# Optimization experiments

Measured on AMD Instinct MI355X. Metric: run time of the kernel, lower is better.

Reference implementation:

```python
import jax, jax.numpy as jnp
import numpy as np

D_MODEL = 1024
NHEAD = 16
HEAD_DIM = D_MODEL // NHEAD
SCALE = 1.0 / np.sqrt(HEAD_DIM).astype(np.float32)
B, L = 2, 2048
NEG_INF = -1e30


def setup_inputs() -> dict:
    key = jax.random.key(0)
    ks = jax.random.split(key, 12)
    xav = np.sqrt(6.0 / (D_MODEL + D_MODEL)).astype(np.float32)  # xavier_uniform gain=1
    def lin_w(k):
        return jax.random.uniform(k, (D_MODEL, D_MODEL), jnp.float32, -xav, xav)
    x = jax.random.normal(ks[0], (B, L, D_MODEL), jnp.float32)
    role_mask = jax.random.randint(ks[1], (B, L), 0, 2, jnp.int32)
    # causal attention mask: True = masked (upper triangle above diagonal)
    attn_mask = jnp.triu(jnp.ones((L, L), jnp.bool_), k=1)
    # random key padding: True = padded key
    key_padding_mask = jax.random.randint(ks[2], (B, L), 0, 2, jnp.int32).astype(jnp.bool_)
    return {
        "x": x,
        "role_mask": role_mask,
        "attn_mask": attn_mask,
        "key_padding_mask": key_padding_mask,
        "Wq": lin_w(ks[3]), "bq": jnp.zeros((D_MODEL,), jnp.float32),
        "Wk": lin_w(ks[4]), "bk": jnp.zeros((D_MODEL,), jnp.float32),
        "Wv": lin_w(ks[5]), "bv": jnp.zeros((D_MODEL,), jnp.float32),
        "Wo": lin_w(ks[6]), "bo": jnp.zeros((D_MODEL,), jnp.float32),
        "delta": jnp.asarray(1.0, jnp.float32),
    }


def reference(x, role_mask, attn_mask, key_padding_mask,
              Wq, bq, Wk, bk, Wv, bv, Wo, bo, delta):
    Bb, Ll, Dd = x.shape
    def heads(t):  # [B,L,D] -> [B,H,L,hd]
        return t.reshape(Bb, Ll, NHEAD, HEAD_DIM).transpose(0, 2, 1, 3)
    Q = heads(x @ Wq.T + bq)
    K = heads(x @ Wk.T + bk)
    V = heads(x @ Wv.T + bv)
    scores = jnp.einsum('bhqd,bhkd->bhqk', Q, K) * SCALE  # [B,H,L,L]
    same_role = (role_mask[:, :, None] == role_mask[:, None, :])  # [B,L,L]
    scores = scores + (same_role.astype(scores.dtype) * delta)[:, None, :, :]
    scores = jnp.where(attn_mask[None, None, :, :], -jnp.inf, scores)
    scores = jnp.where(key_padding_mask[:, None, None, :], -jnp.inf, scores)
    attn = jax.nn.softmax(scores, axis=-1)
    attn = jnp.nan_to_num(attn, nan=0.0, posinf=0.0, neginf=0.0)
    out = jnp.einsum('bhqk,bhkd->bhqd', attn, V)
    out = out.transpose(0, 2, 1, 3).reshape(Bb, Ll, Dd)
    return out @ Wo.T + bo
```

## Files before the change

### kernel.cpp

```cpp
#include <hip/hip_runtime.h>
#include <hip/hip_bf16.h>

#define DM 1024
#define NH 16
#define HD 64
#define BB 2
#define LL 2048
#define SCALE 0.125f
#define NEG_BIG -1e30f
#define LOG2E 1.4426950408889634f
#define SC2 (SCALE * LOG2E)
#define FIXM 16.0f
#define SLOTB 8448
#define POOL0_SLOTS 960

typedef __bf16 bf16;
typedef __bf16 bf16x8 __attribute__((ext_vector_type(8)));
typedef __bf16 bf16x4 __attribute__((ext_vector_type(4)));
typedef float f32x4 __attribute__((ext_vector_type(4)));

static __device__ inline bf16x8 load8(const bf16* p) {
    return *reinterpret_cast<const bf16x8*>(p);
}

static __device__ inline float scrub(float x) {
    union { float f; unsigned u; } c; c.f = x;
    return ((c.u & 0x7F800000u) == 0x7F800000u) ? 0.f : x;
}

typedef __attribute__((address_space(1))) const unsigned char ga_t;
typedef __attribute__((address_space(3))) unsigned char ls_t;
static __device__ inline void gload_lds16(const void* g, void* l) {
    __builtin_amdgcn_global_load_lds((ga_t*)g, (ls_t*)l, 16, 0, 0);
}

__global__ __launch_bounds__(256) void prep_all(
    const float* __restrict__ x,
    const float* __restrict__ Wq, const float* __restrict__ Wk,
    const float* __restrict__ Wv, const float* __restrict__ Wo,
    bf16* __restrict__ xb, bf16* __restrict__ Wqb, bf16* __restrict__ Wkb,
    bf16* __restrict__ Wvb, bf16* __restrict__ Wob,
    const int* __restrict__ role, const void* __restrict__ kpad,
    const float* __restrict__ deltap, float2* __restrict__ biasG)
{
    const int tid = threadIdx.x;
    const int gid = blockIdx.x;
    if (gid < 2048) {
        const float* src; bf16* dst; size_t base;
        if (gid < 1024) { src = x; dst = xb; base = (size_t)gid * 1024; }
        else {
            const int wsel = (gid - 1024) >> 8;
            src = (wsel == 0) ? Wq : (wsel == 1) ? Wk : (wsel == 2) ? Wv : Wo;
            dst = (wsel == 0) ? Wqb : (wsel == 1) ? Wkb : (wsel == 2) ? Wvb : Wob;
            base = (size_t)((gid - 1024) & 255) * 1024;
        }
#pragma unroll
        for (int it = 0; it < 4; it++) {
            const size_t i = base + it * 256 + tid;
            const f32x4 v = ((const f32x4*)src)[i];
            bf16x4 o;
            o[0] = (bf16)v[0]; o[1] = (bf16)v[1]; o[2] = (bf16)v[2]; o[3] = (bf16)v[3];
            ((bf16x4*)dst)[i] = o;
        }
        return;
    }
    const unsigned char* kb = (const unsigned char*)kpad;
    int f3F = 0, fLow = 0, fOff = 0;
    for (int i = (tid & 63); i < BB * LL; i += 64) {
        const unsigned char v = kb[i];
        if (v == 0x3F) f3F = 1;
        if ((i & 3) < 2 && v) fLow = 1;
        if ((i & 3) && v) fOff = 1;
    }
    const int mode = __any(f3F) ? (__any(fLow) ? 3 : 2) : (__any(fOff) ? 1 : 0);
    const float d2 = scrub(deltap[0]) * LOG2E;
    const int idx = (gid - 2048) * 256 + tid;
    const bool pad = (mode == 0) ? (((const int*)kpad)[idx] != 0)
                   : (mode == 1) ? (((const unsigned char*)kpad)[idx] != 0)
                   : (mode == 2) ? (((const float*)kpad)[idx] != 0.f)
                                 : (((const unsigned short*)kpad)[idx] != 0);
    const int r = role[idx];
    const float base = (pad ? NEG_BIG : 0.f) - FIXM;
    float2 o;
    o.x = base + ((r == 0) ? d2 : 0.f);
    o.y = base + ((r == 1) ? d2 : 0.f);
    biasG[idx] = o;
}

__global__ __launch_bounds__(256) void qkv_bf16(
    const bf16* __restrict__ xb,
    const bf16* __restrict__ Wqb, const bf16* __restrict__ Wkb, const bf16* __restrict__ Wvb,
    const float* __restrict__ bq, const float* __restrict__ bk, const float* __restrict__ bv,
    bf16* __restrict__ qw, bf16* __restrict__ kw, bf16* __restrict__ vtw)
{
    __shared__ bf16 As[128 * 32];
    __shared__ bf16 Bs[128 * 32];
    const int tid = threadIdx.x;
    const int lane = tid & 63, w = tid >> 6;
    const int wm = w >> 1, wn = w & 1;
    const int ln = lane & 15, quad = lane >> 4;

    const int m0 = blockIdx.x * 128;
    const int sel = blockIdx.y >> 3;
    const int nloc0 = (blockIdx.y & 7) * 128;

    const bf16* Wb = (sel == 0) ? Wqb : ((sel == 1) ? Wkb : Wvb);
    const float* bias = (sel == 0) ? bq : ((sel == 1) ? bk : bv);

    const int rA = lane >> 2;
    const int cA = (lane & 3) * 8;

    f32x4 acc[4][4] = {};
    for (int k0 = 0; k0 < DM; k0 += 32) {
        __syncthreads();
#pragma unroll
        for (int s = 0; s < 2; s++) {
            const int r0 = s * 64 + w * 16;
            gload_lds16(xb + (size_t)(m0 + r0 + rA) * DM + k0 + cA, &As[r0 * 32]);
            gload_lds16(Wb + (size_t)(nloc0 + r0 + rA) * DM + k0 + cA, &Bs[r0 * 32]);
        }
        __syncthreads();
        bf16x8 a[4], b[4];
#pragma unroll
        for (int mi = 0; mi < 4; mi++)
            a[mi] = *(bf16x8*)&As[(wm * 64 + mi * 16 + ln) * 32 + quad * 8];
#pragma unroll
        for (int ni = 0; ni < 4; ni++)
            b[ni] = *(bf16x8*)&Bs[(wn * 64 + ni * 16 + ln) * 32 + quad * 8];
#pragma unroll
        for (int mi = 0; mi < 4; mi++)
#pragma unroll
            for (int ni = 0; ni < 4; ni++)
                acc[mi][ni] = __builtin_amdgcn_mfma_f32_16x16x32_bf16(a[mi], b[ni], acc[mi][ni], 0, 0, 0);
    }

#pragma unroll
    for (int mi = 0; mi < 4; mi++) {
#pragma unroll
        for (int ni = 0; ni < 4; ni++) {
            const int ncol = nloc0 + wn * 64 + ni * 16 + ln;
            const float bv_ = bias[ncol];
            const int hh = ncol >> 6, dd = ncol & 63;
#pragma unroll
            for (int i = 0; i < 4; i++) {
                const int row = m0 + wm * 64 + mi * 16 + quad * 4 + i;
                const int bb = row >> 11, llr = row & (LL - 1);
                const bf16 v = (bf16)scrub(acc[mi][ni][i] + bv_);
                if (sel == 0)
                    qw[(((size_t)(bb * NH + hh) * LL) + llr) * HD + dd] = v;
                else if (sel == 1)
                    kw[(((size_t)(bb * NH + hh) * LL) + llr) * HD + dd] = v;
                else {
                    const int kl = llr & 63;
                    const int pos = (llr & ~63) + ((kl & 15) * 4 + (kl >> 4));
                    vtw[(((size_t)(bb * NH + hh) * HD) + dd) * LL + pos] = v;
                }
            }
        }
    }
}

#define PSTR 36
__global__ __launch_bounds__(256) void attn_v9(
    const bf16* __restrict__ qw, const bf16* __restrict__ kw, const bf16* __restrict__ vtw,
    const int* __restrict__ role, const float2* __restrict__ biasG,
    char* __restrict__ pool0, char* __restrict__ pool1,
    bf16* __restrict__ attn_out)
{
    const int xg = blockIdx.x;
    int qb, c;
    if (xg < 24)      { qb = 31 - xg / 3; c = xg % 3; }
    else if (xg < 48) { qb = 23 - (xg - 24) / 2; c = (xg - 24) % 2; }
    else              { qb = 59 - xg; c = 0; }
    const int nch = (qb + 12) / 12;

    __shared__ bf16 Ks[2][2][64 * 32];
    __shared__ bf16 Vs[2][2][64 * 32];
    __shared__ bf16 Ps[4][2][16 * PSTR];

    const int tid = threadIdx.x;
    const int lane = tid & 63, w = tid >> 6;
    const int col = lane & 15, quad = lane >> 4;
    const int bh = blockIdx.y;
    const int h = bh & (NH - 1), b = bh >> 4;
    const int q0 = qb * 64 + w * 16;

    const bf16* qbase = qw + (size_t)((b * NH + h) * LL) * HD;
    const bf16* kbase = kw + (size_t)((b * NH + h) * LL) * HD;
    const bf16* vbase = vtw + (size_t)((b * NH + h) * HD) * LL;
    const float2* bias2 = biasG + (size_t)b * LL;
    const int* rrow = role + b * LL;

    const int srow = lane >> 2;
    const int scol = (lane & 3) * 8;
    const bf16* ksrc = kbase + (size_t)(w * 16 + srow) * HD + scol;
    const bf16* vsrc = vbase + (size_t)(w * 16 + srow) * LL + scol;

    bf16x8 qf[2];
    qf[0] = load8(qbase + (size_t)(q0 + col) * HD + quad * 8);
    qf[1] = load8(qbase + (size_t)(q0 + col) * HD + 32 + quad * 8);

    int role_q[4];
#pragma unroll
    for (int i = 0; i < 4; i++) role_q[i] = rrow[q0 + quad * 4 + i];

    float lacc[4] = {0.f, 0.f, 0.f, 0.f};
    f32x4 o[4] = {};

    const int t0 = c * 12;
    const int t1 = (t0 + 12 < qb + 1) ? t0 + 12 : qb + 1;

    {
        const int kp = t0 * 64;
#pragma unroll
        for (int st = 0; st < 2; st++)
            gload_lds16(ksrc + (size_t)kp * HD + st * 32, &Ks[0][st][w * 512]);
#pragma unroll
        for (int kh = 0; kh < 2; kh++)
            gload_lds16(vsrc + kp + kh * 32, &Vs[0][kh][w * 512]);
    }

    for (int kt = t0; kt < t1; kt++) {
        const int cur = (kt - t0) & 1;
        __syncthreads();

        if (kt + 1 < t1) {
            const int k1 = (kt + 1) * 64;
#pragma unroll
            for (int st = 0; st < 2; st++)
                gload_lds16(ksrc + (size_t)k1 * HD + st * 32, &Ks[cur ^ 1][st][w * 512]);
#pragma unroll
            for (int kh = 0; kh < 2; kh++)
                gload_lds16(vsrc + k1 + kh * 32, &Vs[cur ^ 1][kh][w * 512]);
        }

        const int k0 = kt * 64;
        float2 bb[4];
#pragma unroll
        for (int ns = 0; ns < 4; ns++) bb[ns] = bias2[k0 + ns * 16 + col];

        f32x4 s[4] = {};
#pragma unroll
        for (int st = 0; st < 2; st++) {
#pragma unroll
            for (int ns = 0; ns < 4; ns++) {
                const bf16x8 kf = *(bf16x8*)&Ks[cur][st][(ns * 16 + col) * 32 + quad * 8];
                s[ns] = __builtin_amdgcn_mfma_f32_16x16x32_bf16(qf[st], kf, s[ns], 0, 0, 0);
            }
        }
        const bool diag = (kt == qb);
        const int half = col >> 3;
        const int poff = (col & 7) * 4;
#pragma unroll
        for (int i = 0; i < 4; i++) {
            bf16x4 pk;
#pragma unroll
            for (int ns = 0; ns < 4; ns++) {
                float sv = fmaf(s[ns][i], SC2, role_q[i] ? bb[ns].y : bb[ns].x);
                if (diag && (k0 + ns * 16 + col) > q0 + quad * 4 + i) sv = NEG_BIG;
                const float p = exp2f(fminf(sv, 14.f));
                lacc[i] += p;
                pk[ns] = (bf16)p;
            }
            *(bf16x4*)&Ps[w][half][(quad * 4 + i) * PSTR + poff] = pk;
        }
        bf16x8 pf[2];
#pragma unroll
        for (int st = 0; st < 2; st++)
            pf[st] = *(bf16x8*)&Ps[w][st][col * PSTR + quad * 8];
#pragma unroll
        for (int ns = 0; ns < 4; ns++) {
#pragma unroll
            for (int kh = 0; kh < 2; kh++) {
                const bf16x8 vf = *(bf16x8*)&Vs[cur][kh][(ns * 16 + col) * 32 + quad * 8];
                o[ns] = __builtin_amdgcn_mfma_f32_16x16x32_bf16(pf[kh], vf, o[ns], 0, 0, 0);
            }
        }
    }

    if (nch == 1) {
        bf16* orow = attn_out + (size_t)(b * LL) * DM;
#pragma unroll
        for (int i = 0; i < 4; i++) {
            float l = lacc[i];
#pragma unroll
            for (int off = 8; off > 0; off >>= 1)
                l += __shfl_xor(l, off, 16);
            const float inv = (l > 0.f) ? 1.f / l : 0.f;
            const int qq = q0 + quad * 4 + i;
#pragma unroll
            for (int ns = 0; ns < 4; ns++)
                orow[(size_t)qq * DM + h * HD + ns * 16 + col] = (bf16)scrub(o[ns][i] * inv);
        }
    } else {
        const int base = (qb <= 23) ? (qb - 12) * 2 : 24 + (qb - 24) * 3;
        const int slot = bh * 48 + base + c;
        char* ptr = (slot < POOL0_SLOTS) ? (pool0 + (size_t)slot * SLOTB)
                                         : (pool1 + (size_t)(slot - POOL0_SLOTS) * SLOTB);
        bf16* op = (bf16*)ptr;
        float* lp = (float*)(ptr + 8192);
#pragma unroll
        for (int i = 0; i < 4; i++) {
            float l = lacc[i];
#pragma unroll
            for (int off = 8; off > 0; off >>= 1)
                l += __shfl_xor(l, off, 16);
            const int r = w * 16 + quad * 4 + i;
            if (col == 0) lp[r] = l;
#pragma unroll
            for (int ns = 0; ns < 4; ns++)
                op[r * 64 + ns * 16 + col] = (bf16)scrub(o[ns][i]);
        }
    }
}

__global__ __launch_bounds__(256) void combine(
    const char* __restrict__ pool0, const char* __restrict__ pool1,
    bf16* __restrict__ attn_out)
{
    const int qb = 12 + blockIdx.x;
    const int bh = blockIdx.y;
    const int h = bh & (NH - 1), b = bh >> 4;
    const int nch = (qb + 12) / 12;
    const int base = (qb <= 23) ? (qb - 12) * 2 : 24 + (qb - 24) * 3;

    const char* ptr[3];
    for (int c = 0; c < nch; c++) {
        const int slot = bh * 48 + base + c;
        ptr[c] = (slot < POOL0_SLOTS) ? (pool0 + (size_t)slot * SLOTB)
                                      : (pool1 + (size_t)(slot - POOL0_SLOTS) * SLOTB);
    }

    __shared__ float linv[64];
    const int tid = threadIdx.x;
    if (tid < 64) {
        float ls = 0.f;
        for (int c = 0; c < nch; c++) ls += ((const float*)(ptr[c] + 8192))[tid];
        linv[tid] = (ls > 0.f) ? 1.f / ls : 0.f;
    }
    __syncthreads();

    const int r = tid >> 2;
    const int d0 = (tid & 3) * 16;
    float acc[16] = {};
    for (int c = 0; c < nch; c++) {
        const bf16* op = (const bf16*)ptr[c];
#pragma unroll
        for (int half = 0; half < 2; half++) {
            const bf16x8 v = load8(op + r * 64 + d0 + half * 8);
#pragma unroll
            for (int j = 0; j < 8; j++) acc[half * 8 + j] += (float)v[j];
        }
    }
    const float inv = linv[r];
    bf16x8 outv[2];
#pragma unroll
    for (int half = 0; half < 2; half++)
#pragma unroll
        for (int j = 0; j < 8; j++)
            outv[half][j] = (bf16)scrub(acc[half * 8 + j] * inv);
    bf16* orow = attn_out + ((size_t)(b * LL) + qb * 64 + r) * DM + h * HD + d0;
    *(bf16x8*)orow = outv[0];
    *(bf16x8*)(orow + 8) = outv[1];
}

__global__ __launch_bounds__(256) void out_bf16(
    const bf16* __restrict__ A, const bf16* __restrict__ Wb,
    const float* __restrict__ bias, float* __restrict__ out)
{
    __shared__ bf16 As[128 * 32];
    __shared__ bf16 Bs[64 * 32];
    const int tid = threadIdx.x;
    const int lane = tid & 63, w = tid >> 6;
    const int ln = lane & 15, quad = lane >> 4;
    const int m0 = blockIdx.x * 128;
    const int n0 = blockIdx.y * 64;

    const int rA = lane >> 2;
    const int cA = (lane & 3) * 8;

    f32x4 acc[2][4] = {};
    for (int k0 = 0; k0 < DM; k0 += 32) {
        __syncthreads();
#pragma unroll
        for (int s = 0; s < 2; s++) {
            const int r0 = s * 64 + w * 16;
            gload_lds16(A + (size_t)(m0 + r0 + rA) * DM + k0 + cA, &As[r0 * 32]);
        }
        gload_lds16(Wb + (size_t)(n0 + w * 16 + rA) * DM + k0 + cA, &Bs[w * 16 * 32]);
        __syncthreads();
        bf16x8 a[2], b[4];
#pragma unroll
        for (int mi = 0; mi < 2; mi++)
            a[mi] = *(bf16x8*)&As[(w * 32 + mi * 16 + ln) * 32 + quad * 8];
#pragma unroll
        for (int ni = 0; ni < 4; ni++)
            b[ni] = *(bf16x8*)&Bs[(ni * 16 + ln) * 32 + quad * 8];
#pragma unroll
        for (int mi = 0; mi < 2; mi++)
#pragma unroll
            for (int ni = 0; ni < 4; ni++)
                acc[mi][ni] = __builtin_amdgcn_mfma_f32_16x16x32_bf16(a[mi], b[ni], acc[mi][ni], 0, 0, 0);
    }
#pragma unroll
    for (int mi = 0; mi < 2; mi++) {
#pragma unroll
        for (int ni = 0; ni < 4; ni++) {
            const int ncol = n0 + ni * 16 + ln;
            const float bv_ = bias[ncol];
#pragma unroll
            for (int i = 0; i < 4; i++) {
                const int row = m0 + w * 32 + mi * 16 + quad * 4 + i;
                out[(size_t)row * DM + ncol] = scrub(acc[mi][ni][i] + bv_);
            }
        }
    }
}

extern "C" void kernel_launch(void* const* d_in, const int* in_sizes, int n_in,
                              void* d_out, int out_size, void* d_ws, size_t ws_size,
                              hipStream_t stream) {
    const float* x    = (const float*)d_in[0];
    const int*   role = (const int*)d_in[1];
    const void*  kpad = d_in[3];
    const float* Wq = (const float*)d_in[4];
    const float* bq = (const float*)d_in[5];
    const float* Wk = (const float*)d_in[6];
    const float* bk = (const float*)d_in[7];
    const float* Wv = (const float*)d_in[8];
    const float* bv = (const float*)d_in[9];
    const float* Wo = (const float*)d_in[10];
    const float* bo = (const float*)d_in[11];
    const float* dl = (const float*)d_in[12];

    char* ws = (char*)d_ws;
    bf16* qw   = (bf16*)(ws);
    bf16* kw   = (bf16*)(ws + (size_t)(8u  << 20));
    bf16* Wqb  = (bf16*)(ws + (size_t)(16u << 20));
    bf16* Wkb  = (bf16*)(ws + (size_t)(18u << 20));
    bf16* Wvb  = (bf16*)(ws + (size_t)(20u << 20));
    char* pool0 = ws + (size_t)(16u << 20);
    bf16* aw   = (bf16*)(ws + (size_t)(24u << 20));
    bf16* vtw  = (bf16*)(ws + (size_t)(32u << 20));
    bf16* xb   = (bf16*)(ws + (size_t)(40u << 20));
    char* pool1 = ws + (size_t)(40u << 20);
    bf16* Wob  = (bf16*)(ws + (size_t)(48u << 20) + 65536);
    float2* biasG = (float2*)(ws + (size_t)(48u << 20));
    float* out = (float*)d_out;

    prep_all<<<dim3(2064), dim3(256), 0, stream>>>(
        x, Wq, Wk, Wv, Wo, xb, Wqb, Wkb, Wvb, Wob, role, kpad, dl, biasG);
    qkv_bf16<<<dim3(32, 24), dim3(256), 0, stream>>>(
        xb, Wqb, Wkb, Wvb, bq, bk, bv, qw, kw, vtw);
    attn_v9<<<dim3(60, 32), dim3(256), 0, stream>>>(
        qw, kw, vtw, role, biasG, pool0, pool1, aw);
    combine<<<dim3(20, 32), dim3(256), 0, stream>>>(pool0, pool1, aw);
    out_bf16<<<dim3(32, 16), dim3(256), 0, stream>>>(aw, Wob, bo, out);
}
```

Baseline: 246.3 us.

## Fuse split-KV combine into attention via atomic tickets and XOR-swizzle LDS tiles

Removes the separate combine kernel. Each split-KV attention block now takes an atomic ticket, and the last block to finish for a query tile reduces the partial outputs and writes the normalized result. The tickets are zeroed in the prep kernel. Separately, LDS tiles in the QKV GEMM, the output GEMM and the attention K/V staging use an XOR swizzle of the 16-byte column chunk by row, meant to cut bank conflicts on the MFMA fragment reads. This saves one launch and its tail, at the cost of threadfences and atomics in the attention kernel.

```diff
diff --git a/kernel.cpp b/kernel.cpp
--- a/kernel.cpp
+++ b/kernel.cpp
@@ -34,6 +34,7 @@
     __builtin_amdgcn_global_load_lds((ga_t*)g, (ls_t*)l, 16, 0, 0);
 }
 
+
 __global__ __launch_bounds__(256) void prep_all(
     const float* __restrict__ x,
     const float* __restrict__ Wq, const float* __restrict__ Wk,
@@ -41,7 +42,8 @@
     bf16* __restrict__ xb, bf16* __restrict__ Wqb, bf16* __restrict__ Wkb,
     bf16* __restrict__ Wvb, bf16* __restrict__ Wob,
     const int* __restrict__ role, const void* __restrict__ kpad,
-    const float* __restrict__ deltap, float2* __restrict__ biasG)
+    const float* __restrict__ deltap, float2* __restrict__ biasG,
+    int* __restrict__ tickets)
 {
     const int tid = threadIdx.x;
     const int gid = blockIdx.x;
@@ -75,6 +77,7 @@
     const int mode = __any(f3F) ? (__any(fLow) ? 3 : 2) : (__any(fOff) ? 1 : 0);
     const float d2 = scrub(deltap[0]) * LOG2E;
     const int idx = (gid - 2048) * 256 + tid;
+    if (idx < 640) tickets[idx] = 0;
     const bool pad = (mode == 0) ? (((const int*)kpad)[idx] != 0)
                    : (mode == 1) ? (((const unsigned char*)kpad)[idx] != 0)
                    : (mode == 2) ? (((const float*)kpad)[idx] != 0.f)
@@ -108,7 +111,7 @@
     const float* bias = (sel == 0) ? bq : ((sel == 1) ? bk : bv);
 
     const int rA = lane >> 2;
-    const int cA = (lane & 3) * 8;
+    const int cA = (((lane & 3) ^ (rA & 3)) * 8);
 
     f32x4 acc[4][4] = {};
     for (int k0 = 0; k0 < DM; k0 += 32) {
@@ -122,11 +125,15 @@
         __syncthreads();
         bf16x8 a[4], b[4];
 #pragma unroll
-        for (int mi = 0; mi < 4; mi++)
-            a[mi] = *(bf16x8*)&As[(wm * 64 + mi * 16 + ln) * 32 + quad * 8];
-#pragma unroll
-        for (int ni = 0; ni < 4; ni++)
-            b[ni] = *(bf16x8*)&Bs[(wn * 64 + ni * 16 + ln) * 32 + quad * 8];
+        for (int mi = 0; mi < 4; mi++) {
+            const int row = wm * 64 + mi * 16 + ln;
+            a[mi] = *(bf16x8*)&As[row * 32 + ((quad ^ (row & 3)) * 8)];
+        }
+#pragma unroll
+        for (int ni = 0; ni < 4; ni++) {
+            const int row = wn * 64 + ni * 16 + ln;
+            b[ni] = *(bf16x8*)&Bs[row * 32 + ((quad ^ (row & 3)) * 8)];
+        }
 #pragma unroll
         for (int mi = 0; mi < 4; mi++)
 #pragma unroll
@@ -161,10 +168,11 @@
 }
 
 #define PSTR 36
-__global__ __launch_bounds__(256) void attn_v9(
+__global__ __launch_bounds__(256) void attn_v10(
     const bf16* __restrict__ qw, const bf16* __restrict__ kw, const bf16* __restrict__ vtw,
     const int* __restrict__ role, const float2* __restrict__ biasG,
     char* __restrict__ pool0, char* __restrict__ pool1,
+    int* __restrict__ tickets,
     bf16* __restrict__ attn_out)
 {
     const int xg = blockIdx.x;
@@ -177,6 +185,8 @@
     __shared__ bf16 Ks[2][2][64 * 32];
     __shared__ bf16 Vs[2][2][64 * 32];
     __shared__ bf16 Ps[4][2][16 * PSTR];
+    __shared__ float linv[64];
+    __shared__ int amLast;
 
     const int tid = threadIdx.x;
     const int lane = tid & 63, w = tid >> 6;
@@ -192,7 +202,7 @@
     const int* rrow = role + b * LL;
 
     const int srow = lane >> 2;
-    const int scol = (lane & 3) * 8;
+    const int scol = (((lane & 3) ^ (srow & 3)) * 8);
     const bf16* ksrc = kbase + (size_t)(w * 16 + srow) * HD + scol;
     const bf16* vsrc = vbase + (size_t)(w * 16 + srow) * LL + scol;
 
@@ -244,7 +254,8 @@
         for (int st = 0; st < 2; st++) {
 #pragma unroll
             for (int ns = 0; ns < 4; ns++) {
-                const bf16x8 kf = *(bf16x8*)&Ks[cur][st][(ns * 16 + col) * 32 + quad * 8];
+                const int row = ns * 16 + col;
+                const bf16x8 kf = *(bf16x8*)&Ks[cur][st][row * 32 + ((quad ^ (row & 3)) * 8)];
                 s[ns] = __builtin_amdgcn_mfma_f32_16x16x32_bf16(qf[st], kf, s[ns], 0, 0, 0);
             }
         }
@@ -272,7 +283,8 @@
         for (int ns = 0; ns < 4; ns++) {
 #pragma unroll
             for (int kh = 0; kh < 2; kh++) {
-                const bf16x8 vf = *(bf16x8*)&Vs[cur][kh][(ns * 16 + col) * 32 + quad * 8];
+                const int row = ns * 16 + col;
+                const bf16x8 vf = *(bf16x8*)&Vs[cur][kh][row * 32 + ((quad ^ (row & 3)) * 8)];
                 o[ns] = __builtin_amdgcn_mfma_f32_16x16x32_bf16(pf[kh], vf, o[ns], 0, 0, 0);
             }
         }
@@ -292,9 +304,12 @@
             for (int ns = 0; ns < 4; ns++)
                 orow[(size_t)qq * DM + h * HD + ns * 16 + col] = (bf16)scrub(o[ns][i] * inv);
         }
-    } else {
-        const int base = (qb <= 23) ? (qb - 12) * 2 : 24 + (qb - 24) * 3;
-        const int slot = bh * 48 + base + c;
+        return;
+    }
+
+    const int sbase = (qb <= 23) ? (qb - 12) * 2 : 24 + (qb - 24) * 3;
+    {
+        const int slot = bh * 48 + sbase + c;
         char* ptr = (slot < POOL0_SLOTS) ? (pool0 + (size_t)slot * SLOTB)
                                          : (pool1 + (size_t)(slot - POOL0_SLOTS) * SLOTB);
         bf16* op = (bf16*)ptr;
@@ -312,53 +327,45 @@
                 op[r * 64 + ns * 16 + col] = (bf16)scrub(o[ns][i]);
         }
     }
-}
-
-__global__ __launch_bounds__(256) void combine(
-    const char* __restrict__ pool0, const char* __restrict__ pool1,
-    bf16* __restrict__ attn_out)
-{
-    const int qb = 12 + blockIdx.x;
-    const int bh = blockIdx.y;
-    const int h = bh & (NH - 1), b = bh >> 4;
-    const int nch = (qb + 12) / 12;
-    const int base = (qb <= 23) ? (qb - 12) * 2 : 24 + (qb - 24) * 3;
+
+    __threadfence();
+    if (tid == 0)
+        amLast = (atomicAdd(&tickets[(qb - 12) * 32 + bh], 1) == nch - 1);
+    __syncthreads();
+    if (!amLast) return;
+    __threadfence();
 
     const char* ptr[3];
-    for (int c = 0; c < nch; c++) {
-        const int slot = bh * 48 + base + c;
-        ptr[c] = (slot < POOL0_SLOTS) ? (pool0 + (size_t)slot * SLOTB)
-                                      : (pool1 + (size_t)(slot - POOL0_SLOTS) * SLOTB);
-    }
-
-    __shared__ float linv[64];
-    const int tid = threadIdx.x;
+    for (int cc = 0; cc < nch; cc++) {
+        const int slot = bh * 48 + sbase + cc;
+        ptr[cc] = (slot < POOL0_SLOTS) ? (pool0 + (size_t)slot * SLOTB)
+                                       : (pool1 + (size_t)(slot - POOL0_SLOTS) * SLOTB);
+    }
     if (tid < 64) {
         float ls = 0.f;
-        for (int c = 0; c < nch; c++) ls += ((const float*)(ptr[c] + 8192))[tid];
+        for (int cc = 0; cc < nch; cc++) ls += ((const float*)(ptr[cc] + 8192))[tid];
         linv[tid] = (ls > 0.f) ? 1.f / ls : 0.f;
     }
     __syncthreads();
-
     const int r = tid >> 2;
     const int d0 = (tid & 3) * 16;
     float acc[16] = {};
-    for (int c = 0; c < nch; c++) {
-        const bf16* op = (const bf16*)ptr[c];
-#pragma unroll
-        for (int half = 0; half < 2; half++) {
-            const bf16x8 v = load8(op + r * 64 + d0 + half * 8);
-#pragma unroll
-            for (int j = 0; j < 8; j++) acc[half * 8 + j] += (float)v[j];
+    for (int cc = 0; cc < nch; cc++) {
+        const bf16* op = (const bf16*)ptr[cc];
+#pragma unroll
+        for (int hf = 0; hf < 2; hf++) {
+            const bf16x8 v = load8(op + r * 64 + d0 + hf * 8);
+#pragma unroll
+            for (int j = 0; j < 8; j++) acc[hf * 8 + j] += (float)v[j];
         }
     }
     const float inv = linv[r];
     bf16x8 outv[2];
 #pragma unroll
-    for (int half = 0; half < 2; half++)
+    for (int hf = 0; hf < 2; hf++)
 #pragma unroll
         for (int j = 0; j < 8; j++)
-            outv[half][j] = (bf16)scrub(acc[half * 8 + j] * inv);
+            outv[hf][j] = (bf16)scrub(acc[hf * 8 + j] * inv);
     bf16* orow = attn_out + ((size_t)(b * LL) + qb * 64 + r) * DM + h * HD + d0;
     *(bf16x8*)orow = outv[0];
     *(bf16x8*)(orow + 8) = outv[1];
@@ -377,7 +384,7 @@
     const int n0 = blockIdx.y * 64;
 
     const int rA = lane >> 2;
-    const int cA = (lane & 3) * 8;
+    const int cA = (((lane & 3) ^ (rA & 3)) * 8);
 
     f32x4 acc[2][4] = {};
     for (int k0 = 0; k0 < DM; k0 += 32) {
@@ -391,11 +398,15 @@
         __syncthreads();
         bf16x8 a[2], b[4];
 #pragma unroll
-        for (int mi = 0; mi < 2; mi++)
-            a[mi] = *(bf16x8*)&As[(w * 32 + mi * 16 + ln) * 32 + quad * 8];
-#pragma unroll
-        for (int ni = 0; ni < 4; ni++)
-            b[ni] = *(bf16x8*)&Bs[(ni * 16 + ln) * 32 + quad * 8];
+        for (int mi = 0; mi < 2; mi++) {
+            const int row = w * 32 + mi * 16 + ln;
+            a[mi] = *(bf16x8*)&As[row * 32 + ((quad ^ (row & 3)) * 8)];
+        }
+#pragma unroll
+        for (int ni = 0; ni < 4; ni++) {
+            const int row = ni * 16 + ln;
+            b[ni] = *(bf16x8*)&Bs[row * 32 + ((quad ^ (row & 3)) * 8)];
+        }
 #pragma unroll
         for (int mi = 0; mi < 2; mi++)
 #pragma unroll
@@ -444,16 +455,16 @@
     bf16* vtw  = (bf16*)(ws + (size_t)(32u << 20));
     bf16* xb   = (bf16*)(ws + (size_t)(40u << 20));
     char* pool1 = ws + (size_t)(40u << 20);
+    float2* biasG = (float2*)(ws + (size_t)(48u << 20));
+    int* tickets  = (int*)(ws + (size_t)(48u << 20) + 32768);
     bf16* Wob  = (bf16*)(ws + (size_t)(48u << 20) + 65536);
-    float2* biasG = (float2*)(ws + (size_t)(48u << 20));
     float* out = (float*)d_out;
 
     prep_all<<<dim3(2064), dim3(256), 0, stream>>>(
-        x, Wq, Wk, Wv, Wo, xb, Wqb, Wkb, Wvb, Wob, role, kpad, dl, biasG);
+        x, Wq, Wk, Wv, Wo, xb, Wqb, Wkb, Wvb, Wob, role, kpad, dl, biasG, tickets);
     qkv_bf16<<<dim3(32, 24), dim3(256), 0, stream>>>(
         xb, Wqb, Wkb, Wvb, bq, bk, bv, qw, kw, vtw);
-    attn_v9<<<dim3(60, 32), dim3(256), 0, stream>>>(
-        qw, kw, vtw, role, biasG, pool0, pool1, aw);
-    combine<<<dim3(20, 32), dim3(256), 0, stream>>>(pool0, pool1, aw);
+    attn_v10<<<dim3(60, 32), dim3(256), 0, stream>>>(
+        qw, kw, vtw, role, biasG, pool0, pool1, tickets, aw);
     out_bf16<<<dim3(32, 16), dim3(256), 0, stream>>>(aw, Wob, bo, out);
 }
```

Result: slower. 551.7 us (+124.0%).
